# Optimization experiments

Measured on AMD Instinct MI355X. Metric: run time of the kernel, lower is better.

Reference implementation:

```python
import jax, jax.numpy as jnp
import numpy as np

B, S, D, H = 2, 2048, 1024, 16
HD = D // H  # head_dim = 64
ROPE_BASE = 10000.0
NEG = -1e9


def rope_cos_sin(seq_len, head_dim, dtype):
    inv_freq = 1.0 / (ROPE_BASE ** (jnp.arange(0, head_dim, 2, dtype=jnp.float32) / head_dim))
    t = jnp.arange(seq_len, dtype=jnp.float32)
    freqs = jnp.outer(t, inv_freq)              # [S, HD/2]
    emb = jnp.concatenate([freqs, freqs], axis=-1)  # [S, HD]
    return jnp.cos(emb).astype(dtype), jnp.sin(emb).astype(dtype)


def rotate_half(x):
    half = x.shape[-1] // 2
    return jnp.concatenate([-x[..., half:], x[..., :half]], axis=-1)


def setup_inputs() -> dict:
    key = jax.random.key(0)
    ks = jax.random.split(key, 9)
    s = 0.02
    x = jax.random.normal(ks[0], (B, S, D), dtype=jnp.float32)
    # additive causal mask: 0 on/below diagonal, -1e9 above
    mask = jnp.where(jnp.tril(jnp.ones((S, S), dtype=bool)), 0.0, NEG).astype(jnp.float32)
    params = {
        'Wq': jax.random.normal(ks[1], (D, D), jnp.float32) * s,
        'bq': jnp.zeros((D,), jnp.float32),
        'Wk': jax.random.normal(ks[2], (D, D), jnp.float32) * s,
        'bk': jnp.zeros((D,), jnp.float32),
        'Wv': jax.random.normal(ks[3], (D, D), jnp.float32) * s,
        'bv': jnp.zeros((D,), jnp.float32),
        'Wo': jax.random.normal(ks[4], (D, D), jnp.float32) * s,
        'bo': jnp.zeros((D,), jnp.float32),
    }
    return {'x': x, 'mask': mask, **params}


def reference(x, mask, Wq, bq, Wk, bk, Wv, bv, Wo, bo):
    Bv, Sv, Dv = x.shape
    q = (x @ Wq + bq).reshape(Bv, Sv, H, HD).transpose(0, 2, 1, 3)  # [B,H,S,HD]
    k = (x @ Wk + bk).reshape(Bv, Sv, H, HD).transpose(0, 2, 1, 3)
    v = (x @ Wv + bv).reshape(Bv, Sv, H, HD).transpose(0, 2, 1, 3)
    cos, sin = rope_cos_sin(Sv, HD, x.dtype)      # [S, HD]
    cos = cos[None, None]                          # [1,1,S,HD]
    sin = sin[None, None]
    q = q * cos + rotate_half(q) * sin
    k = k * cos + rotate_half(k) * sin
    scale = jnp.asarray(np.sqrt(HD), x.dtype)
    scores = jnp.einsum('bhqd,bhkd->bhqk', q, k) / scale  # [B,H,S,S]
    scores = scores + mask[None, None]
    attn = jax.nn.softmax(scores, axis=-1)
    out = jnp.einsum('bhqk,bhkd->bhqd', attn, v)   # [B,H,S,HD]
    out = out.transpose(0, 2, 1, 3).reshape(Bv, Sv, Dv)
    return out @ Wo + bo
```

## Files before the change

### kernel.cpp

```cpp
#include <hip/hip_runtime.h>
#include <hip/hip_bf16.h>
#include <cstdint>

typedef __bf16 bf16;
typedef __bf16 bf16x4 __attribute__((ext_vector_type(4)));
typedef __bf16 bf16x8 __attribute__((ext_vector_type(8)));
typedef float f32x4 __attribute__((ext_vector_type(4)));

#define DEV __device__ __forceinline__

DEV void gl_lds16(const void* g, void* l) {
    __builtin_amdgcn_global_load_lds(
        (__attribute__((address_space(1))) void*)(uintptr_t)g,
        (__attribute__((address_space(3))) void*)(uint32_t)(uintptr_t)l,
        16, 0, 0);
}

DEV f32x4 mfma16(bf16x8 a, bf16x8 b, f32x4 c) {
    return __builtin_amdgcn_mfma_f32_16x16x32_bf16(a, b, c, 0, 0, 0);
}


__global__ void cvt_x(const float* __restrict__ x, bf16* __restrict__ xb) {
    const int i = blockIdx.x * 256 + threadIdx.x;
    const float4 v = ((const float4*)x)[i];
    bf16x4 o = {(bf16)v.x, (bf16)v.y, (bf16)v.z, (bf16)v.w};
    *(bf16x4*)(xb + (size_t)i * 4) = o;
}

__global__ void wtrans(const float* __restrict__ w0, const float* __restrict__ w1,
                       const float* __restrict__ w2, const float* __restrict__ w3,
                       bf16* __restrict__ WT) {
    __shared__ float t[32][33];
    const float* W = blockIdx.z == 0 ? w0 : blockIdx.z == 1 ? w1 : blockIdx.z == 2 ? w2 : w3;
    bf16* dst = WT + (size_t)blockIdx.z * 1024 * 1024;
    const int tx = threadIdx.x, ty = threadIdx.y;
    const int kb = blockIdx.x * 32, nb = blockIdx.y * 32;
#pragma unroll
    for (int i = 0; i < 4; ++i)
        t[ty + i * 8][tx] = W[(size_t)(kb + ty + i * 8) * 1024 + nb + tx];
    __syncthreads();
#pragma unroll
    for (int i = 0; i < 4; ++i)
        dst[(size_t)(nb + ty + i * 8) * 1024 + kb + tx] = (bf16)t[tx][ty + i * 8];
}

__global__ void rope_tab(float* __restrict__ cosT, float* __restrict__ sinT) {
    const int t = blockIdx.x * 256 + threadIdx.x;
    const int s = t >> 6, i = t & 31;
    const float inv = expf(-(float)i * (9.210340371976184f / 32.0f));
    const float ang = (float)s * inv;
    cosT[t] = cosf(ang);
    sinT[t] = sinf(ang);
}

template <int MODE>
__global__ __launch_bounds__(256) void gemm_k(
    const bf16* __restrict__ A, const bf16* __restrict__ BT,
    const float* __restrict__ bias0, const float* __restrict__ bias1,
    const float* __restrict__ bias2,
    bf16* __restrict__ outQ, bf16* __restrict__ outK, bf16* __restrict__ outV,
    const float* __restrict__ cosT, const float* __restrict__ sinT,
    float* __restrict__ outF) {
    extern __shared__ char smem[];
    const int tid = threadIdx.x;
    const int lane = tid & 63;
    const int wv = tid >> 6;
    const int wm = wv >> 1, wn = wv & 1;
    const int bm = blockIdx.x, bn = blockIdx.y;
    const int q = lane & 15, g = lane >> 4;

    const bf16* Ab = A + (size_t)bm * 128 * 1024;
    const bf16* Bb = BT + (size_t)bn * 128 * 1024;
    const int r0 = tid >> 2, c0 = (tid & 3) * 8;

    auto stage = [&](int b, int kb) {
        char* base = smem + b * 16384;
        gl_lds16(Ab + (size_t)r0 * 1024 + kb + c0, base + tid * 16);
        gl_lds16(Ab + (size_t)(r0 + 64) * 1024 + kb + c0, base + 4096 + tid * 16);
        gl_lds16(Bb + (size_t)r0 * 1024 + kb + c0, base + 8192 + tid * 16);
        gl_lds16(Bb + (size_t)(r0 + 64) * 1024 + kb + c0, base + 12288 + tid * 16);
    };

    f32x4 acc[4][4] = {};

    stage(0, 0);
    stage(1, 32);
    asm volatile("s_waitcnt vmcnt(4)" ::: "memory");
    __builtin_amdgcn_s_barrier();

    for (int kt = 0; kt < 32; ++kt) {
        if (kt + 2 < 32) stage((kt + 2) % 3, (kt + 2) * 32);
        const bf16* As = (const bf16*)(smem + (kt % 3) * 16384);
        const bf16* Bs = As + 128 * 32;
        bf16x8 af[4], bfr[4];
#pragma unroll
        for (int mi = 0; mi < 4; ++mi)
            af[mi] = *(const bf16x8*)(As + (wm * 64 + mi * 16 + q) * 32 + g * 8);
#pragma unroll
        for (int ni = 0; ni < 4; ++ni)
            bfr[ni] = *(const bf16x8*)(Bs + (wn * 64 + ni * 16 + q) * 32 + g * 8);
#pragma unroll
        for (int mi = 0; mi < 4; ++mi)
#pragma unroll
            for (int ni = 0; ni < 4; ++ni)
                acc[mi][ni] = mfma16(af[mi], bfr[ni], acc[mi][ni]);
        if (kt + 2 < 32) asm volatile("s_waitcnt vmcnt(4)" ::: "memory");
        else             asm volatile("s_waitcnt vmcnt(0)" ::: "memory");
        __builtin_amdgcn_s_barrier();
    }

    const int n0 = bn * 128 + wn * 64;
    if constexpr (MODE == 0) {
        const int seg = n0 >> 10;
        const int nloc = n0 & 1023;
        const int h = nloc >> 6;
        const float* bias = seg == 0 ? bias0 : (seg == 1 ? bias1 : bias2);
        const float qsc = (seg == 0) ? 0.125f : 1.0f;
        float bvv[4];
#pragma unroll
        for (int ni = 0; ni < 4; ++ni) bvv[ni] = bias[nloc + ni * 16 + q];
        if (seg < 2) {
            bf16* dst = seg == 0 ? outQ : outK;
#pragma unroll
            for (int mi = 0; mi < 4; ++mi) {
#pragma unroll
                for (int r = 0; r < 4; ++r) {
                    const int m = bm * 128 + wm * 64 + mi * 16 + g * 4 + r;
                    const int s = m & 2047, bb = m >> 11;
                    const size_t rowb = ((size_t)((bb << 4) | h) * 2048 + s) * 64;
#pragma unroll
                    for (int ni = 0; ni < 4; ++ni) {
                        const int hd = ni * 16 + q;
                        const float c = cosT[s * 64 + hd], sn = sinT[s * 64 + hd];
                        const float v0 = acc[mi][ni][r] + bvv[ni];
                        const float v1 = acc[mi][ni ^ 2][r] + bvv[ni ^ 2];
                        dst[rowb + hd] = (bf16)((v0 * c + (ni < 2 ? -v1 : v1) * sn) * qsc);
                    }
                }
            }
        } else {
            bf16* Tw = (bf16*)smem + wv * (64 * 72);
#pragma unroll
            for (int mi = 0; mi < 4; ++mi)
#pragma unroll
                for (int ni = 0; ni < 4; ++ni)
#pragma unroll
                    for (int r = 0; r < 4; ++r)
                        Tw[(ni * 16 + q) * 72 + mi * 16 + g * 4 + r] =
                            (bf16)(acc[mi][ni][r] + bvv[ni]);
            const int mstart = bm * 128 + wm * 64;
            const int s0 = mstart & 2047, bb = mstart >> 11;
            bf16* vbase = outV + (size_t)((bb << 4) | h) * (64 * 2048);
#pragma unroll
            for (int i = 0; i < 8; ++i) {
                const int row = i * 8 + (lane >> 3);
                const int col = (lane & 7) * 8;
                bf16x8 vvv = *(const bf16x8*)(Tw + row * 72 + col);
                *(bf16x8*)(vbase + (size_t)row * 2048 + s0 + col) = vvv;
            }
        }
    } else {
        float bvv[4];
#pragma unroll
        for (int ni = 0; ni < 4; ++ni) bvv[ni] = bias0[n0 + ni * 16 + q];
#pragma unroll
        for (int mi = 0; mi < 4; ++mi)
#pragma unroll
            for (int r = 0; r < 4; ++r) {
                const int m = bm * 128 + wm * 64 + mi * 16 + g * 4 + r;
#pragma unroll
                for (int ni = 0; ni < 4; ++ni)
                    outF[(size_t)m * 1024 + n0 + ni * 16 + q] = acc[mi][ni][r] + bvv[ni];
            }
    }
}

__global__ __launch_bounds__(512, 2) void attn_k(const bf16* __restrict__ Qr,
                                                 const bf16* __restrict__ Kr,
                                                 const bf16* __restrict__ Vt,
                                                 bf16* __restrict__ AO) {
    const int gid = (int)blockIdx.x;
    const int xcd = gid & 7;
    const int bh = xcd + 8 * ((gid >> 3) & 3);
    const int idx = gid >> 5;
    const int p = idx >> 1;
    const int h = 1 - (idx & 1);
    const int tid = threadIdx.x;
    const int lane = tid & 63, wv = tid >> 6;
    const int q = lane & 15, g = lane >> 4;
    const int qt_w = (wv >> 2) ? p : (15 - p);
    const int q0w = qt_w * 128 + h * 64 + (wv & 3) * 16;
    const int nt = 31 - 2 * p + h;
    const size_t hb = (size_t)bh * (2048 * 64);
    extern __shared__ char smem[];
    bf16* P = (bf16*)(smem + 49152 + wv * 2304);

    const bf16* Kg = Kr + hb;
    const bf16* Vg = Vt + hb;
    const int swz = (q & 7) << 4;

    auto stage = [&](int b, int kb) {
        char* base = smem + b * 16384;
        {
            const int X = tid * 16;
            const int row = X >> 7;
            const int cbg = (X & 127) ^ ((row & 7) << 4);
            gl_lds16(Kg + (size_t)(kb + row) * 64 + (cbg >> 1), base + X);
        }
        {
            const int X = tid * 16;
            const int row = X >> 7;
            const int cbg = (X & 127) ^ ((row & 7) << 4);
            gl_lds16(Vg + (size_t)row * 2048 + kb + (cbg >> 1), base + 8192 + X);
        }
    };

    bf16x8 qf[2];
    {
        const bf16* qp = Qr + hb + (size_t)(q0w + q) * 64 + g * 8;
        qf[0] = *(const bf16x8*)(qp);
        qf[1] = *(const bf16x8*)(qp + 32);
    }
    f32x4 o[4] = {};
    float l_run = 0.0f;
    const f32x4 z4 = {0.f, 0.f, 0.f, 0.f};
    const int rmax = q0w + 15;

    stage(0, 0);
    stage(1, 64);
    asm volatile("s_waitcnt vmcnt(2)" ::: "memory");
    __builtin_amdgcn_s_barrier();

    for (int kt = 0; kt < nt; ++kt) {
        const int kb = kt * 64;
        if (kt + 2 < nt) stage((kt + 2) % 3, kb + 128);
        if (kb <= rmax) {
            char* Kl = smem + (kt % 3) * 16384;
            char* Vl = Kl + 8192;
            f32x4 st[4];
            __builtin_amdgcn_s_setprio(1);
#pragma unroll
            for (int f = 0; f < 4; ++f) {
                const int row = f * 16 + q;
                const bf16x8 k0 = *(const bf16x8*)(Kl + row * 128 + ((g * 16) ^ swz));
                const bf16x8 k1 = *(const bf16x8*)(Kl + row * 128 + ((64 + g * 16) ^ swz));
                f32x4 t0 = mfma16(k0, qf[0], z4);
                st[f] = mfma16(k1, qf[1], t0);
            }
            __builtin_amdgcn_s_setprio(0);
            bf16x8 vf[4][2];
#pragma unroll
            for (int nf = 0; nf < 4; ++nf) {
                const int row = nf * 16 + q;
                vf[nf][0] = *(const bf16x8*)(Vl + row * 128 + ((g * 16) ^ swz));
                vf[nf][1] = *(const bf16x8*)(Vl + row * 128 + ((64 + g * 16) ^ swz));
            }
            const bool maskT = (kb + 63 > q0w);
            float tsum = 0.f;
#pragma unroll
            for (int f = 0; f < 4; ++f)
#pragma unroll
                for (int r = 0; r < 4; ++r) {
                    float sv = st[f][r];
                    if (maskT && (kb + f * 16 + g * 4 + r > q0w + q)) sv = -3.0e38f;
                    const float pv = __expf(fminf(sv, 20.0f));
                    st[f][r] = pv;
                    tsum += pv;
                }
            l_run += tsum;
#pragma unroll
            for (int f = 0; f < 4; ++f) {
                bf16x4 pv = {(bf16)st[f][0], (bf16)st[f][1],
                             (bf16)st[f][2], (bf16)st[f][3]};
                *(bf16x4*)&P[q * 72 + f * 16 + g * 4] = pv;
            }
            __builtin_amdgcn_s_setprio(1);
#pragma unroll
            for (int t = 0; t < 2; ++t) {
                const bf16x8 pa = *(const bf16x8*)&P[q * 72 + t * 32 + g * 8];
#pragma unroll
                for (int nf = 0; nf < 4; ++nf)
                    o[nf] = mfma16(pa, vf[nf][t], o[nf]);
            }
            __builtin_amdgcn_s_setprio(0);
        }
        if (kt + 2 < nt) asm volatile("s_waitcnt vmcnt(2)" ::: "memory");
        else             asm volatile("s_waitcnt vmcnt(0)" ::: "memory");
        __builtin_amdgcn_s_barrier();
    }

    l_run += __shfl_xor(l_run, 16);
    l_run += __shfl_xor(l_run, 32);
    float li[4];
#pragma unroll
    for (int r = 0; r < 4; ++r) li[r] = 1.0f / __shfl(l_run, g * 4 + r);
    const int b_ = bh >> 4, h_ = bh & 15;
#pragma unroll
    for (int nf = 0; nf < 4; ++nf)
#pragma unroll
        for (int r = 0; r < 4; ++r) {
            const int qg = q0w + g * 4 + r;
            AO[(size_t)(b_ * 2048 + qg) * 1024 + h_ * 64 + nf * 16 + q] =
                (bf16)(o[nf][r] * li[r]);
        }
}


extern "C" void kernel_launch(void* const* d_in, const int* in_sizes, int n_in,
                              void* d_out, int out_size, void* d_ws, size_t ws_size,
                              hipStream_t stream) {
    const float* x  = (const float*)d_in[0];
    const float* Wq = (const float*)d_in[2];
    const float* bq = (const float*)d_in[3];
    const float* Wk = (const float*)d_in[4];
    const float* bk = (const float*)d_in[5];
    const float* Wv = (const float*)d_in[6];
    const float* bv = (const float*)d_in[7];
    const float* Wo = (const float*)d_in[8];
    const float* bo = (const float*)d_in[9];
    float* out = (float*)d_out;
    char* ws = (char*)d_ws;
    const size_t MB_ = 1024 * 1024;
    bf16* xb    = (bf16*)(ws);
    bf16* WT    = (bf16*)(ws + 8 * MB_);
    bf16* Qrp   = (bf16*)(ws + 16 * MB_);
    bf16* Krp   = (bf16*)(ws + 24 * MB_);
    bf16* Vt    = (bf16*)(ws + 32 * MB_);
    bf16* AO    = (bf16*)(ws + 40 * MB_);
    float* cosT = (float*)(ws + 48 * MB_);
    float* sinT = (float*)(ws + 48 * MB_ + 512 * 1024);

    cvt_x<<<4096, 256, 0, stream>>>(x, xb);
    wtrans<<<dim3(32, 32, 4), dim3(32, 8), 0, stream>>>(Wq, Wk, Wv, Wo, WT);
    rope_tab<<<512, 256, 0, stream>>>(cosT, sinT);
    gemm_k<0><<<dim3(32, 24), 256, 49152, stream>>>(xb, WT, bq, bk, bv, Qrp, Krp, Vt,
                                                    cosT, sinT, nullptr);
    attn_k<<<dim3(512, 1), 512, 67584, stream>>>(Qrp, Krp, Vt, AO);
    gemm_k<1><<<dim3(32, 8), 256, 49152, stream>>>(AO, WT + (size_t)3072 * 1024, bo,
                                                   nullptr, nullptr, nullptr, nullptr,
                                                   nullptr, nullptr, nullptr, out);
}
```

Baseline: 108.2 us.

## Halve attention block waves and give each wave two 16-row query tiles

The attention kernel now launches 256 threads (4 waves) per block instead of 512, and each wave processes two 16-row query sub-tiles, so every K/V fragment read from LDS feeds twice as many MFMAs. Staging of each K/V tile now takes two loads per thread with adjusted vmcnt waits, and shared memory per block shrinks. The intent is better LDS reuse and less load traffic per MFMA. The cost is higher register pressure and fewer waves per CU to hide latency, with the per-wave P buffer reused serially across the two sub-tiles.

```diff
diff --git a/kernel.cpp b/kernel.cpp
--- a/kernel.cpp
+++ b/kernel.cpp
@@ -176,7 +176,7 @@
     }
 }
 
-__global__ __launch_bounds__(512, 2) void attn_k(const bf16* __restrict__ Qr,
+__global__ __launch_bounds__(256, 2) void attn_k(const bf16* __restrict__ Qr,
                                                  const bf16* __restrict__ Kr,
                                                  const bf16* __restrict__ Vt,
                                                  bf16* __restrict__ AO) {
@@ -189,8 +189,8 @@
     const int tid = threadIdx.x;
     const int lane = tid & 63, wv = tid >> 6;
     const int q = lane & 15, g = lane >> 4;
-    const int qt_w = (wv >> 2) ? p : (15 - p);
-    const int q0w = qt_w * 128 + h * 64 + (wv & 3) * 16;
+    const int qt_w = (wv >> 1) ? p : (15 - p);
+    const int qb = qt_w * 128 + h * 64 + (wv & 1) * 32;
     const int nt = 31 - 2 * p + h;
     const size_t hb = (size_t)bh * (2048 * 64);
     extern __shared__ char smem[];
@@ -202,34 +202,37 @@
 
     auto stage = [&](int b, int kb) {
         char* base = smem + b * 16384;
-        {
-            const int X = tid * 16;
+#pragma unroll
+        for (int i = 0; i < 2; ++i) {
+            const int X = i * 4096 + tid * 16;
             const int row = X >> 7;
             const int cbg = (X & 127) ^ ((row & 7) << 4);
             gl_lds16(Kg + (size_t)(kb + row) * 64 + (cbg >> 1), base + X);
         }
-        {
-            const int X = tid * 16;
+#pragma unroll
+        for (int i = 0; i < 2; ++i) {
+            const int X = i * 4096 + tid * 16;
             const int row = X >> 7;
             const int cbg = (X & 127) ^ ((row & 7) << 4);
             gl_lds16(Vg + (size_t)row * 2048 + kb + (cbg >> 1), base + 8192 + X);
         }
     };
 
-    bf16x8 qf[2];
-    {
-        const bf16* qp = Qr + hb + (size_t)(q0w + q) * 64 + g * 8;
-        qf[0] = *(const bf16x8*)(qp);
-        qf[1] = *(const bf16x8*)(qp + 32);
-    }
-    f32x4 o[4] = {};
-    float l_run = 0.0f;
+    bf16x8 qf[2][2];
+#pragma unroll
+    for (int s = 0; s < 2; ++s) {
+        const bf16* qp = Qr + hb + (size_t)(qb + s * 16 + q) * 64 + g * 8;
+        qf[s][0] = *(const bf16x8*)(qp);
+        qf[s][1] = *(const bf16x8*)(qp + 32);
+    }
+    f32x4 o[2][4] = {};
+    float l_run[2] = {0.0f, 0.0f};
     const f32x4 z4 = {0.f, 0.f, 0.f, 0.f};
-    const int rmax = q0w + 15;
+    const int rmax = qb + 31;
 
     stage(0, 0);
     stage(1, 64);
-    asm volatile("s_waitcnt vmcnt(2)" ::: "memory");
+    asm volatile("s_waitcnt vmcnt(4)" ::: "memory");
     __builtin_amdgcn_s_barrier();
 
     for (int kt = 0; kt < nt; ++kt) {
@@ -238,15 +241,17 @@
         if (kb <= rmax) {
             char* Kl = smem + (kt % 3) * 16384;
             char* Vl = Kl + 8192;
-            f32x4 st[4];
+            f32x4 st[2][4];
             __builtin_amdgcn_s_setprio(1);
 #pragma unroll
             for (int f = 0; f < 4; ++f) {
                 const int row = f * 16 + q;
                 const bf16x8 k0 = *(const bf16x8*)(Kl + row * 128 + ((g * 16) ^ swz));
                 const bf16x8 k1 = *(const bf16x8*)(Kl + row * 128 + ((64 + g * 16) ^ swz));
-                f32x4 t0 = mfma16(k0, qf[0], z4);
-                st[f] = mfma16(k1, qf[1], t0);
+                f32x4 t0 = mfma16(k0, qf[0][0], z4);
+                st[0][f] = mfma16(k1, qf[0][1], t0);
+                f32x4 t1 = mfma16(k0, qf[1][0], z4);
+                st[1][f] = mfma16(k1, qf[1][1], t1);
             }
             __builtin_amdgcn_s_setprio(0);
             bf16x8 vf[4][2];
@@ -256,54 +261,63 @@
                 vf[nf][0] = *(const bf16x8*)(Vl + row * 128 + ((g * 16) ^ swz));
                 vf[nf][1] = *(const bf16x8*)(Vl + row * 128 + ((64 + g * 16) ^ swz));
             }
-            const bool maskT = (kb + 63 > q0w);
-            float tsum = 0.f;
-#pragma unroll
-            for (int f = 0; f < 4; ++f)
-#pragma unroll
-                for (int r = 0; r < 4; ++r) {
-                    float sv = st[f][r];
-                    if (maskT && (kb + f * 16 + g * 4 + r > q0w + q)) sv = -3.0e38f;
-                    const float pv = __expf(fminf(sv, 20.0f));
-                    st[f][r] = pv;
-                    tsum += pv;
+#pragma unroll
+            for (int s = 0; s < 2; ++s) {
+                const int q0s = qb + s * 16;
+                const bool maskT = (kb + 63 > q0s);
+                float tsum = 0.f;
+#pragma unroll
+                for (int f = 0; f < 4; ++f)
+#pragma unroll
+                    for (int r = 0; r < 4; ++r) {
+                        float sv = st[s][f][r];
+                        if (maskT && (kb + f * 16 + g * 4 + r > q0s + q)) sv = -3.0e38f;
+                        const float pv = __expf(fminf(sv, 20.0f));
+                        st[s][f][r] = pv;
+                        tsum += pv;
+                    }
+                l_run[s] += tsum;
+#pragma unroll
+                for (int f = 0; f < 4; ++f) {
+                    bf16x4 pv = {(bf16)st[s][f][0], (bf16)st[s][f][1],
+                                 (bf16)st[s][f][2], (bf16)st[s][f][3]};
+                    *(bf16x4*)&P[q * 72 + f * 16 + g * 4] = pv;
                 }
-            l_run += tsum;
-#pragma unroll
-            for (int f = 0; f < 4; ++f) {
-                bf16x4 pv = {(bf16)st[f][0], (bf16)st[f][1],
-                             (bf16)st[f][2], (bf16)st[f][3]};
-                *(bf16x4*)&P[q * 72 + f * 16 + g * 4] = pv;
-            }
-            __builtin_amdgcn_s_setprio(1);
-#pragma unroll
-            for (int t = 0; t < 2; ++t) {
-                const bf16x8 pa = *(const bf16x8*)&P[q * 72 + t * 32 + g * 8];
-#pragma unroll
-                for (int nf = 0; nf < 4; ++nf)
-                    o[nf] = mfma16(pa, vf[nf][t], o[nf]);
-            }
-            __builtin_amdgcn_s_setprio(0);
+                __builtin_amdgcn_s_setprio(1);
+#pragma unroll
+                for (int t = 0; t < 2; ++t) {
+                    const bf16x8 pa = *(const bf16x8*)&P[q * 72 + t * 32 + g * 8];
+#pragma unroll
+                    for (int nf = 0; nf < 4; ++nf)
+                        o[s][nf] = mfma16(pa, vf[nf][t], o[s][nf]);
+                }
+                __builtin_amdgcn_s_setprio(0);
+            }
         }
-        if (kt + 2 < nt) asm volatile("s_waitcnt vmcnt(2)" ::: "memory");
+        if (kt + 2 < nt) asm volatile("s_waitcnt vmcnt(4)" ::: "memory");
         else             asm volatile("s_waitcnt vmcnt(0)" ::: "memory");
         __builtin_amdgcn_s_barrier();
     }
 
-    l_run += __shfl_xor(l_run, 16);
-    l_run += __shfl_xor(l_run, 32);
-    float li[4];
-#pragma unroll
-    for (int r = 0; r < 4; ++r) li[r] = 1.0f / __shfl(l_run, g * 4 + r);
     const int b_ = bh >> 4, h_ = bh & 15;
 #pragma unroll
-    for (int nf = 0; nf < 4; ++nf)
-#pragma unroll
-        for (int r = 0; r < 4; ++r) {
-            const int qg = q0w + g * 4 + r;
-            AO[(size_t)(b_ * 2048 + qg) * 1024 + h_ * 64 + nf * 16 + q] =
-                (bf16)(o[nf][r] * li[r]);
-        }
+    for (int s = 0; s < 2; ++s) {
+        float lr = l_run[s];
+        lr += __shfl_xor(lr, 16);
+        lr += __shfl_xor(lr, 32);
+        float li[4];
+#pragma unroll
+        for (int r = 0; r < 4; ++r) li[r] = 1.0f / __shfl(lr, g * 4 + r);
+        const int q0s = qb + s * 16;
+#pragma unroll
+        for (int nf = 0; nf < 4; ++nf)
+#pragma unroll
+            for (int r = 0; r < 4; ++r) {
+                const int qg = q0s + g * 4 + r;
+                AO[(size_t)(b_ * 2048 + qg) * 1024 + h_ * 64 + nf * 16 + q] =
+                    (bf16)(o[s][nf][r] * li[r]);
+            }
+    }
 }
 
 
@@ -336,7 +350,7 @@
     rope_tab<<<512, 256, 0, stream>>>(cosT, sinT);
     gemm_k<0><<<dim3(32, 24), 256, 49152, stream>>>(xb, WT, bq, bk, bv, Qrp, Krp, Vt,
                                                     cosT, sinT, nullptr);
-    attn_k<<<dim3(512, 1), 512, 67584, stream>>>(Qrp, Krp, Vt, AO);
+    attn_k<<<dim3(512, 1), 256, 58368, stream>>>(Qrp, Krp, Vt, AO);
     gemm_k<1><<<dim3(32, 8), 256, 49152, stream>>>(AO, WT + (size_t)3072 * 1024, bo,
                                                    nullptr, nullptr, nullptr, nullptr,
                                                    nullptr, nullptr, nullptr, out);
```

Result: slower. 122.2 us (+12.9%).
